# Kernel optimization log

Hardware: AMD Instinct MI355X
Metric: run time of the kernel (lower is better)

## Reference

```python
import jax, jax.numpy as jnp
import numpy as np

# CIM / quantization constants hardcoded in the source module
INPUT_BIT = 8
WEIGHT_BIT = 4
OUTPUT_BIT = 8
DAC_BIT = 2
ADC_BIT = 8
ADC_GAIN_1_SCALE = 1.0 / 63.0
GAIN_MIN, GAIN_MAX = 1.0, 255.0
N_SLICES = INPUT_BIT // DAC_BIT  # 4 bit-serial input slices of 2 bits each


def ste_round(v):
    # straight-through round: forward = round(v), backward = identity
    return v + jax.lax.stop_gradient(jnp.round(v) - v)


def conv2d(x, w):
    # NCHW conv, stride 1, padding k//2 (SAME for odd k)
    return jax.lax.conv_general_dilated(
        x, w, window_strides=(1, 1), padding='SAME',
        dimension_numbers=('NCHW', 'OIHW', 'NCHW'))


def setup_inputs() -> dict:
    key = jax.random.key(0)
    kx, kw, kb = jax.random.split(key, 3)
    B, Cin, H, W = 16, 4, 512, 512
    Cout, K = 8, 3
    x = jax.random.uniform(kx, (B, Cin, H, W), dtype=jnp.float32)  # non-negative activations
    weight = jax.random.normal(kw, (Cout, Cin, K, K), dtype=jnp.float32) * 0.05
    bias = jax.random.normal(kb, (Cout,), dtype=jnp.float32) * 0.01
    s_in = jnp.float32(1.0 / 255.0)   # LSQ input scale (8-bit unsigned)
    s_w = jnp.float32(0.02)           # LSQ weight scale (4-bit signed)
    s_out = jnp.float32(0.05)         # LSQ output scale (8-bit signed)
    return {"x": x, "weight": weight, "bias": bias,
            "s_in": s_in, "s_w": s_w, "s_out": s_out}


def reference(x, weight, bias, s_in, s_w, s_out):
    in_max = 2.0 ** INPUT_BIT - 1.0          # 255
    w_lim = 2.0 ** (WEIGHT_BIT - 1) - 1.0    # 7
    adc_max = 2.0 ** (ADC_BIT - 1) - 1.0     # 127
    o_lim = 2.0 ** (OUTPUT_BIT - 1) - 1.0    # 127
    base = float(2 ** DAC_BIT)               # 4 levels per DAC slice

    # LSQ quantization of input (unsigned) and weight (signed), STE rounding
    xq = jnp.clip(ste_round(x / s_in), 0.0, in_max)        # integer-valued floats
    wq = jnp.clip(ste_round(weight / s_w), -w_lim, w_lim)

    # ideal integer conv (gradient path)
    ideal = conv2d(xq, wq)

    # bit-serial DAC/ADC CIM path (forward only; noise_scale=0 so no noise)
    xi = jax.lax.stop_gradient(xq)
    wi = jax.lax.stop_gradient(wq)
    psums = []
    for s in range(N_SLICES):
        sl = jnp.mod(jnp.floor(xi / (base ** s)), base)    # 2-bit slice in [0,3]
        psums.append(conv2d(sl, wi))
    # ADC gain adjustment ('gain' mode): integer gain in [1,255], LSB = 1/(gain*gain_1_scale)
    p_absmax = jnp.maximum(
        jnp.max(jnp.stack([jnp.max(jnp.abs(p)) for p in psums])), 1e-6)
    gain = jnp.clip(jnp.round(adc_max / (p_absmax * ADC_GAIN_1_SCALE)),
                    GAIN_MIN, GAIN_MAX)
    step = 1.0 / (gain * ADC_GAIN_1_SCALE)
    acc = jnp.zeros_like(ideal)
    for s, p in enumerate(psums):
        adc_out = jnp.clip(jnp.round(p / step), -adc_max, adc_max) * step
        acc = acc + adc_out * (base ** s)

    # straight-through: forward uses analog path, backward uses ideal conv
    psum = ideal + jax.lax.stop_gradient(acc - ideal)

    out = psum * (s_in * s_w) + bias[None, :, None, None]
    # LSQ output quantization (8-bit signed)
    out = jnp.clip(ste_round(out / s_out), -o_lim, o_lim) * s_out
    return out
```

## Files before the change

### kernel.cpp

```cpp
#include <hip/hip_runtime.h>
#include <stdint.h>

#define B_   16
#define CIN  4
#define COUT 8
#define H_   512
#define W_   512
#define HP   (H_ + 2)
#define WP   (W_ + 2)
#define PMAX 756
#define TBL  (2 * PMAX + 1)
#define RPB  8
#define GY   (H_ / RPB)
#define NBLK (2 * GY * B_)
#define NQ   (B_ * HP)

__device__ __forceinline__ int dot4(uint32_t a, int b, int c) {
#if __has_builtin(__builtin_amdgcn_sdot4)
    return __builtin_amdgcn_sdot4((int)a, b, c, false);
#else
    int r = c;
#pragma unroll
    for (int i = 0; i < 4; ++i) {
        int av = (int)((a >> (8 * i)) & 0xFFu);
        int bv = ((int)(((uint32_t)b) << (24 - 8 * i))) >> 24;
        r += av * bv;
    }
    return r;
#endif
}

__device__ __forceinline__ int dot8(uint32_t a, int b, int c) {
#if __has_builtin(__builtin_amdgcn_sdot8)
    return __builtin_amdgcn_sdot8((int)a, b, c, false);
#else
    int r = c;
#pragma unroll
    for (int i = 0; i < 8; ++i) {
        int av = (int)((a >> (4 * i)) & 0xFu);
        int bv = ((int)(((uint32_t)b) << (28 - 4 * i))) >> 28;
        r += av * bv;
    }
    return r;
#endif
}

__device__ __forceinline__ float rfl_f(float v) {
    return __int_as_float(__builtin_amdgcn_readfirstlane(__float_as_int(v)));
}

__device__ __forceinline__ int wquant(const float* w, float s_w,
                                      int co, int ci, int tap) {
    const int kh = tap / 3, kw = tap % 3;
    float wv = w[((co * CIN + ci) * 3 + kh) * 3 + kw];
    float q  = rintf(__fdiv_rn(wv, s_w));
    q = fminf(fmaxf(q, -7.0f), 7.0f);
    return (int)q;
}

__global__ __launch_bounds__(128) void quant_pack_kernel(
        const float* __restrict__ x, const float* __restrict__ weight,
        const float* __restrict__ s_in_p, const float* __restrict__ s_w_p,
        uint32_t* __restrict__ xq, uint32_t* __restrict__ wq8,
        int* __restrict__ absmax) {
    const int raw = blockIdx.x;
    const int lin = (raw & 7) * (NQ / 8) + (raw >> 3);
    const int b = lin / HP, hp = lin % HP;
    const int t = threadIdx.x;
    if (raw == 0) {
        if (t == 0) *absmax = 0;
        const float s_w = *s_w_p;
        if (t < 32) {
            const int co = t >> 2, p = t & 3;
            const int tA = (p == 0) ? 0 : (p == 1) ? 3 : (p == 2) ? 6 : 2;
            const int tB = (p == 0) ? 1 : (p == 1) ? 4 : (p == 2) ? 7 : 5;
            uint32_t v = 0;
#pragma unroll
            for (int ci = 0; ci < CIN; ++ci) {
                v |= ((uint32_t)(wquant(weight, s_w, co, ci, tA) & 0xF)) << (8 * ci);
                v |= ((uint32_t)(wquant(weight, s_w, co, ci, tB) & 0xF)) << (8 * ci + 4);
            }
            wq8[t] = v;
        } else if (t < 40) {
            const int co = t - 32;
            uint32_t v = 0;
#pragma unroll
            for (int ci = 0; ci < CIN; ++ci)
                v |= ((uint32_t)(wquant(weight, s_w, co, ci, 8) & 0xFF)) << (8 * ci);
            wq8[32 + co] = v;
        }
    }
    uint32_t* dst = xq + ((size_t)b * HP + hp) * WP;
    if (hp == 0 || hp == HP - 1) {
        for (int i = t; i < WP; i += 128) dst[i] = 0;
        return;
    }
    const float s_in = *s_in_p;
    const int h = hp - 1;
    const size_t plane = (size_t)H_ * W_;
    const float* xr = x + ((size_t)b * CIN) * plane + (size_t)h * W_ + 4 * t;
    float4 v0 = *(const float4*)(xr);
    float4 v1 = *(const float4*)(xr + plane);
    float4 v2 = *(const float4*)(xr + 2 * plane);
    float4 v3 = *(const float4*)(xr + 3 * plane);
    uint32_t o0 = 0, o1 = 0, o2 = 0, o3 = 0;
#define QP(f, ci, oj)                                                  \
    { float q = rintf(__fdiv_rn((f), s_in));                           \
      q = fminf(fmaxf(q, 0.0f), 255.0f);                               \
      oj |= ((uint32_t)(int)q) << (8 * (ci)); }
    QP(v0.x, 0, o0) QP(v0.y, 0, o1) QP(v0.z, 0, o2) QP(v0.w, 0, o3)
    QP(v1.x, 1, o0) QP(v1.y, 1, o1) QP(v1.z, 1, o2) QP(v1.w, 1, o3)
    QP(v2.x, 2, o0) QP(v2.y, 2, o1) QP(v2.z, 2, o2) QP(v2.w, 2, o3)
    QP(v3.x, 3, o0) QP(v3.y, 3, o1) QP(v3.z, 3, o2) QP(v3.w, 3, o3)
#undef QP
    uint32_t* d = dst + 1 + 4 * t;
    d[0] = o0; d[1] = o1; d[2] = o2; d[3] = o3;
    if (t == 0) dst[0] = 0;
    if (t == 127) dst[WP - 1] = 0;
}

template <int PASS>
__global__ __launch_bounds__(256, 8) void conv_kernel(
        const uint32_t* __restrict__ xq, const uint32_t* __restrict__ wq8,
        const float* __restrict__ bias, const float* __restrict__ sp_in,
        const float* __restrict__ sp_w, const float* __restrict__ sp_out,
        int* __restrict__ absmax, float* __restrict__ out) {
    __shared__ float tbl[PASS == 2 ? TBL : 1];
    __shared__ int   red[PASS == 1 ? 4 : 1];
    const int tid = threadIdx.x;

    int w8s[32], w4s[8];
    {
        const int4* q4 = (const int4*)wq8;
#pragma unroll
        for (int i = 0; i < 8; ++i) {
            int4 w4i = q4[i];
            w8s[4 * i + 0] = __builtin_amdgcn_readfirstlane(w4i.x);
            w8s[4 * i + 1] = __builtin_amdgcn_readfirstlane(w4i.y);
            w8s[4 * i + 2] = __builtin_amdgcn_readfirstlane(w4i.z);
            w8s[4 * i + 3] = __builtin_amdgcn_readfirstlane(w4i.w);
        }
        int4 a0 = q4[8], a1 = q4[9];
        w4s[0] = __builtin_amdgcn_readfirstlane(a0.x);
        w4s[1] = __builtin_amdgcn_readfirstlane(a0.y);
        w4s[2] = __builtin_amdgcn_readfirstlane(a0.z);
        w4s[3] = __builtin_amdgcn_readfirstlane(a0.w);
        w4s[4] = __builtin_amdgcn_readfirstlane(a1.x);
        w4s[5] = __builtin_amdgcn_readfirstlane(a1.y);
        w4s[6] = __builtin_amdgcn_readfirstlane(a1.z);
        w4s[7] = __builtin_amdgcn_readfirstlane(a1.w);
    }

    float scale = 0.0f, s_out = 0.0f, br[COUT];
    if (PASS == 2) {
        const float pabs = fmaxf((float)(*absmax), 1e-6f);
        const float c63  = 1.0f / 63.0f;
        float g = rintf(__fdiv_rn(127.0f, __fmul_rn(pabs, c63)));
        g = fminf(fmaxf(g, 1.0f), 255.0f);
        const float step = __fdiv_rn(1.0f, __fmul_rn(g, c63));
        for (int i = tid; i < TBL; i += 256) {
            float p = (float)(i - PMAX);
            float r = rintf(__fdiv_rn(p, step));
            r = fminf(fmaxf(r, -127.0f), 127.0f);
            tbl[i] = __fmul_rn(r, step);
        }
        scale = __fmul_rn(rfl_f(*sp_in), rfl_f(*sp_w));
        s_out = rfl_f(*sp_out);
#pragma unroll
        for (int co = 0; co < COUT; ++co) br[co] = rfl_f(bias[co]);
        __syncthreads();
    }

    const int raw = blockIdx.x;
    const int lin = (raw & 7) * (NBLK / 8) + (raw >> 3);
    const int bx = lin & 1;
    const int hy = (lin >> 1) & (GY - 1);
    const int b  = lin >> 7;
    const int w0 = bx * 256 + tid;
    const int h0 = hy * RPB;

    const uint32_t* base = xq + ((size_t)b * HP + h0) * WP + w0;
    const size_t plane = (size_t)H_ * W_;

    uint32_t cpA[4][4];
    uint32_t sgl[4][4];

#define EXTROW(slot, v0, v1, v2)                                          \
    do {                                                                  \
        uint32_t lo = ((v0) & 0x0F0F0F0Fu) | (((v1) << 4) & 0xF0F0F0F0u); \
        uint32_t hi = (((v0) >> 4) & 0x0F0F0F0Fu) | ((v1) & 0xF0F0F0F0u); \
        cpA[slot][0] = lo & 0x33333333u;                                  \
        cpA[slot][1] = (lo >> 2) & 0x33333333u;                           \
        cpA[slot][2] = hi & 0x33333333u;                                  \
        cpA[slot][3] = (hi >> 2) & 0x33333333u;                           \
        sgl[slot][0] = (v2) & 0x03030303u;                                \
        sgl[slot][1] = ((v2) >> 2) & 0x03030303u;                         \
        sgl[slot][2] = ((v2) >> 4) & 0x03030303u;                         \
        sgl[slot][3] = ((v2) >> 6) & 0x03030303u;                         \
    } while (0)

    {
        uint32_t r0 = base[0], r1 = base[1], r2 = base[2];
        EXTROW(0, r0, r1, r2);
        r0 = base[WP]; r1 = base[WP + 1]; r2 = base[WP + 2];
        EXTROW(1, r0, r1, r2);
        r0 = base[2 * WP]; r1 = base[2 * WP + 1]; r2 = base[2 * WP + 2];
        EXTROW(2, r0, r1, r2);
    }
    uint32_t n0 = base[3 * WP], n1 = base[3 * WP + 1], n2 = base[3 * WP + 2];

    int runMax = 0, runMin = 0;

#pragma unroll
    for (int s = 0; s < RPB; ++s) {
        if (s >= 1) {
            EXTROW((s + 2) & 3, n0, n1, n2);
            if (s <= RPB - 2) {
                const uint32_t* nr = base + (size_t)(s + 3) * WP;
                n0 = nr[0]; n1 = nr[1]; n2 = nr[2];
            }
        }
        const int m0 = s & 3, m1 = (s + 1) & 3, m2 = (s + 2) & 3;

        uint32_t pc[4];
#pragma unroll
        for (int k = 0; k < 4; ++k) pc[k] = sgl[m0][k] | (sgl[m1][k] << 4);

        float* orow = (PASS == 2)
            ? out + ((size_t)b * COUT * H_ + (size_t)(h0 + s)) * W_ + w0
            : (float*)0;

#pragma unroll
        for (int co = 0; co < COUT; ++co) {
            float of = 0.0f;
#pragma unroll
            for (int k = 0; k < 4; ++k) {
                int a = dot4(sgl[m2][k], w4s[co], 0);
                a = dot8(cpA[m0][k], w8s[co * 4 + 0], a);
                a = dot8(cpA[m1][k], w8s[co * 4 + 1], a);
                a = dot8(cpA[m2][k], w8s[co * 4 + 2], a);
                a = dot8(pc[k],      w8s[co * 4 + 3], a);
                if (PASS == 1) {
                    runMax = max(runMax, a);
                    runMin = min(runMin, a);
                } else {
                    const float v = tbl[a + PMAX];
                    if (k == 0)      of = v;
                    else if (k == 1) of = __fadd_rn(of, __fmul_rn(v, 4.0f));
                    else if (k == 2) of = __fadd_rn(of, __fmul_rn(v, 16.0f));
                    else             of = __fadd_rn(of, __fmul_rn(v, 64.0f));
                }
            }
            if (PASS == 2) {
                float o = __fadd_rn(__fmul_rn(of, scale), br[co]);
                float q = rintf(__fdiv_rn(o, s_out));
                q = fminf(fmaxf(q, -127.0f), 127.0f);
                orow[(size_t)co * plane] = __fmul_rn(q, s_out);
            }
        }
    }
#undef EXTROW

    if (PASS == 1) {
        int m = max(runMax, -runMin);
#pragma unroll
        for (int off = 1; off < 64; off <<= 1)
            m = max(m, __shfl_xor(m, off));
        if ((tid & 63) == 0) red[tid >> 6] = m;
        __syncthreads();
        if (tid == 0) {
            int mm = max(max(red[0], red[1]), max(red[2], red[3]));
            atomicMax(absmax, mm);
        }
    }
}

extern "C" void kernel_launch(void* const* d_in, const int* in_sizes, int n_in,
                              void* d_out, int out_size, void* d_ws, size_t ws_size,
                              hipStream_t stream) {
    const float* x      = (const float*)d_in[0];
    const float* weight = (const float*)d_in[1];
    const float* bias   = (const float*)d_in[2];
    const float* s_in   = (const float*)d_in[3];
    const float* s_w    = (const float*)d_in[4];
    const float* s_out  = (const float*)d_in[5];
    float* out = (float*)d_out;

    int*      absmax = (int*)d_ws;
    uint32_t* wq8    = (uint32_t*)((char*)d_ws + 256);
    uint32_t* xq     = (uint32_t*)((char*)d_ws + 1024);

    quant_pack_kernel<<<dim3(NQ), dim3(128), 0, stream>>>(
        x, weight, s_in, s_w, xq, wq8, absmax);

    conv_kernel<1><<<dim3(NBLK), dim3(256), 0, stream>>>(
        xq, wq8, bias, s_in, s_w, s_out, absmax, out);
    conv_kernel<2><<<dim3(NBLK), dim3(256), 0, stream>>>(
        xq, wq8, bias, s_in, s_w, s_out, absmax, out);
}
```

Measured before the change: 99.10 us.

## Fuse input quantization with first conv pass using LDS tiles

Merges the quantize/pack kernel and the absmax conv pass into one kernel. Each block quantizes a haloed 10-row tile into LDS, writes the packed rows to the workspace for the second pass, and computes the absmax conv directly from LDS. This drops a kernel launch and the global re-read of packed inputs in pass one. In exchange, halo pixels are quantized redundantly, strided scalar loads of x replace float4 loads, and a memset is added to reset absmax.

```diff
diff --git a/kernel.cpp b/kernel.cpp
--- a/kernel.cpp
+++ b/kernel.cpp
@@ -13,7 +13,7 @@
 #define RPB  8
 #define GY   (H_ / RPB)
 #define NBLK (2 * GY * B_)
-#define NQ   (B_ * HP)
+#define LCOL 264
 
 __device__ __forceinline__ int dot4(uint32_t a, int b, int c) {
 #if __has_builtin(__builtin_amdgcn_sdot4)
@@ -58,75 +58,162 @@
     return (int)q;
 }
 
-__global__ __launch_bounds__(128) void quant_pack_kernel(
+__device__ __forceinline__ uint32_t qpix(const float* __restrict__ x,
+                                         float s_in, int b, int d, int c) {
+    const size_t plane = (size_t)H_ * W_;
+    const float* p = x + ((size_t)b * CIN) * plane + (size_t)d * W_ + c;
+    uint32_t v = 0;
+#pragma unroll
+    for (int ci = 0; ci < CIN; ++ci) {
+        float q = rintf(__fdiv_rn(p[ci * plane], s_in));
+        q = fminf(fmaxf(q, 0.0f), 255.0f);
+        v |= ((uint32_t)(int)q) << (8 * ci);
+    }
+    return v;
+}
+
+#define EXTROW(slot, v0, v1, v2)                                          \
+    do {                                                                  \
+        uint32_t lo = ((v0) & 0x0F0F0F0Fu) | (((v1) << 4) & 0xF0F0F0F0u); \
+        uint32_t hi = (((v0) >> 4) & 0x0F0F0F0Fu) | ((v1) & 0xF0F0F0F0u); \
+        cpA[slot][0] = lo & 0x33333333u;                                  \
+        cpA[slot][1] = (lo >> 2) & 0x33333333u;                           \
+        cpA[slot][2] = (hi)&0x33333333u;                                  \
+        cpA[slot][3] = (hi >> 2) & 0x33333333u;                           \
+        sgl[slot][0] = (v2)&0x03030303u;                                  \
+        sgl[slot][1] = ((v2) >> 2) & 0x03030303u;                         \
+        sgl[slot][2] = ((v2) >> 4) & 0x03030303u;                         \
+        sgl[slot][3] = ((v2) >> 6) & 0x03030303u;                         \
+    } while (0)
+
+__global__ __launch_bounds__(256, 8) void quant_conv1(
         const float* __restrict__ x, const float* __restrict__ weight,
         const float* __restrict__ s_in_p, const float* __restrict__ s_w_p,
         uint32_t* __restrict__ xq, uint32_t* __restrict__ wq8,
         int* __restrict__ absmax) {
+    __shared__ uint32_t lds[10][LCOL];
+    __shared__ uint32_t wlds[40];
+    __shared__ int      red[4];
+    const int t = threadIdx.x;
+
     const int raw = blockIdx.x;
-    const int lin = (raw & 7) * (NQ / 8) + (raw >> 3);
-    const int b = lin / HP, hp = lin % HP;
-    const int t = threadIdx.x;
-    if (raw == 0) {
-        if (t == 0) *absmax = 0;
+    const int lin = (raw & 7) * (NBLK / 8) + (raw >> 3);
+    const int bx = lin & 1;
+    const int hy = (lin >> 1) & (GY - 1);
+    const int b  = lin >> 7;
+    const int w0 = bx * 256;
+    const int h0 = hy * RPB;
+
+    const float s_in = *s_in_p;
+
+    if (t < 40) {
         const float s_w = *s_w_p;
+        uint32_t v = 0;
         if (t < 32) {
             const int co = t >> 2, p = t & 3;
             const int tA = (p == 0) ? 0 : (p == 1) ? 3 : (p == 2) ? 6 : 2;
             const int tB = (p == 0) ? 1 : (p == 1) ? 4 : (p == 2) ? 7 : 5;
-            uint32_t v = 0;
 #pragma unroll
             for (int ci = 0; ci < CIN; ++ci) {
                 v |= ((uint32_t)(wquant(weight, s_w, co, ci, tA) & 0xF)) << (8 * ci);
                 v |= ((uint32_t)(wquant(weight, s_w, co, ci, tB) & 0xF)) << (8 * ci + 4);
             }
-            wq8[t] = v;
-        } else if (t < 40) {
+        } else {
             const int co = t - 32;
-            uint32_t v = 0;
 #pragma unroll
             for (int ci = 0; ci < CIN; ++ci)
                 v |= ((uint32_t)(wquant(weight, s_w, co, ci, 8) & 0xFF)) << (8 * ci);
-            wq8[32 + co] = v;
-        }
-    }
-    uint32_t* dst = xq + ((size_t)b * HP + hp) * WP;
-    if (hp == 0 || hp == HP - 1) {
-        for (int i = t; i < WP; i += 128) dst[i] = 0;
-        return;
-    }
-    const float s_in = *s_in_p;
-    const int h = hp - 1;
-    const size_t plane = (size_t)H_ * W_;
-    const float* xr = x + ((size_t)b * CIN) * plane + (size_t)h * W_ + 4 * t;
-    float4 v0 = *(const float4*)(xr);
-    float4 v1 = *(const float4*)(xr + plane);
-    float4 v2 = *(const float4*)(xr + 2 * plane);
-    float4 v3 = *(const float4*)(xr + 3 * plane);
-    uint32_t o0 = 0, o1 = 0, o2 = 0, o3 = 0;
-#define QP(f, ci, oj)                                                  \
-    { float q = rintf(__fdiv_rn((f), s_in));                           \
-      q = fminf(fmaxf(q, 0.0f), 255.0f);                               \
-      oj |= ((uint32_t)(int)q) << (8 * (ci)); }
-    QP(v0.x, 0, o0) QP(v0.y, 0, o1) QP(v0.z, 0, o2) QP(v0.w, 0, o3)
-    QP(v1.x, 1, o0) QP(v1.y, 1, o1) QP(v1.z, 1, o2) QP(v1.w, 1, o3)
-    QP(v2.x, 2, o0) QP(v2.y, 2, o1) QP(v2.z, 2, o2) QP(v2.w, 2, o3)
-    QP(v3.x, 3, o0) QP(v3.y, 3, o1) QP(v3.z, 3, o2) QP(v3.w, 3, o3)
-#undef QP
-    uint32_t* d = dst + 1 + 4 * t;
-    d[0] = o0; d[1] = o1; d[2] = o2; d[3] = o3;
-    if (t == 0) dst[0] = 0;
-    if (t == 127) dst[WP - 1] = 0;
-}
-
-template <int PASS>
-__global__ __launch_bounds__(256, 8) void conv_kernel(
+        }
+        wlds[t] = v;
+        if (raw == 0) wq8[t] = v;
+    }
+
+#pragma unroll 2
+    for (int r = 0; r < 10; ++r) {
+        const int d = h0 - 1 + r;
+        const bool rowok = ((unsigned)d < (unsigned)H_);
+        const int c = w0 - 1 + t;
+        uint32_t v = 0;
+        if (rowok && (unsigned)c < (unsigned)W_) v = qpix(x, s_in, b, d, c);
+        lds[r][t] = v;
+        if (t < 2) {
+            const int c2 = w0 + 255 + t;
+            uint32_t v2 = 0;
+            if (rowok && (unsigned)c2 < (unsigned)W_) v2 = qpix(x, s_in, b, d, c2);
+            lds[r][256 + t] = v2;
+        }
+    }
+    __syncthreads();
+
+    {
+        uint32_t* xb = xq + (size_t)b * HP * WP;
+#pragma unroll
+        for (int r = 1; r <= 8; ++r)
+            xb[(size_t)(h0 + r) * WP + (w0 + 1 + t)] = lds[r][t + 1];
+        if (hy == 0)
+            for (int i = t; i < WP; i += 256) xb[i] = 0;
+        if (hy == GY - 1)
+            for (int i = t; i < WP; i += 256) xb[(size_t)(HP - 1) * WP + i] = 0;
+        if (t == 0) {
+            const int col = (bx == 0) ? 0 : (WP - 1);
+#pragma unroll
+            for (int r = 1; r <= 8; ++r) xb[(size_t)(h0 + r) * WP + col] = 0;
+        }
+    }
+
+    int w8s[32], w4s[8];
+#pragma unroll
+    for (int i = 0; i < 32; ++i)
+        w8s[i] = __builtin_amdgcn_readfirstlane((int)wlds[i]);
+#pragma unroll
+    for (int i = 0; i < 8; ++i)
+        w4s[i] = __builtin_amdgcn_readfirstlane((int)wlds[32 + i]);
+
+    uint32_t cpA[4][4], sgl[4][4];
+    EXTROW(0, lds[0][t], lds[0][t + 1], lds[0][t + 2]);
+    EXTROW(1, lds[1][t], lds[1][t + 1], lds[1][t + 2]);
+
+    int runMax = 0, runMin = 0;
+#pragma unroll
+    for (int s = 0; s < RPB; ++s) {
+        EXTROW((s + 2) & 3, lds[s + 2][t], lds[s + 2][t + 1], lds[s + 2][t + 2]);
+        const int m0 = s & 3, m1 = (s + 1) & 3, m2 = (s + 2) & 3;
+        uint32_t pc[4];
+#pragma unroll
+        for (int k = 0; k < 4; ++k) pc[k] = sgl[m0][k] | (sgl[m1][k] << 4);
+#pragma unroll
+        for (int co = 0; co < COUT; ++co) {
+#pragma unroll
+            for (int k = 0; k < 4; ++k) {
+                int a = dot4(sgl[m2][k], w4s[co], 0);
+                a = dot8(cpA[m0][k], w8s[co * 4 + 0], a);
+                a = dot8(cpA[m1][k], w8s[co * 4 + 1], a);
+                a = dot8(cpA[m2][k], w8s[co * 4 + 2], a);
+                a = dot8(pc[k],      w8s[co * 4 + 3], a);
+                runMax = max(runMax, a);
+                runMin = min(runMin, a);
+            }
+        }
+    }
+
+    int m = max(runMax, -runMin);
+#pragma unroll
+    for (int off = 1; off < 64; off <<= 1)
+        m = max(m, __shfl_xor(m, off));
+    if ((t & 63) == 0) red[t >> 6] = m;
+    __syncthreads();
+    if (t == 0) {
+        int mm = max(max(red[0], red[1]), max(red[2], red[3]));
+        atomicMax(absmax, mm);
+    }
+}
+
+__global__ __launch_bounds__(256, 8) void conv2_kernel(
         const uint32_t* __restrict__ xq, const uint32_t* __restrict__ wq8,
         const float* __restrict__ bias, const float* __restrict__ sp_in,
         const float* __restrict__ sp_w, const float* __restrict__ sp_out,
         int* __restrict__ absmax, float* __restrict__ out) {
-    __shared__ float tbl[PASS == 2 ? TBL : 1];
-    __shared__ int   red[PASS == 1 ? 4 : 1];
+    __shared__ float tbl[TBL];
     const int tid = threadIdx.x;
 
     int w8s[32], w4s[8];
@@ -151,25 +238,23 @@
         w4s[7] = __builtin_amdgcn_readfirstlane(a1.w);
     }
 
-    float scale = 0.0f, s_out = 0.0f, br[COUT];
-    if (PASS == 2) {
-        const float pabs = fmaxf((float)(*absmax), 1e-6f);
-        const float c63  = 1.0f / 63.0f;
-        float g = rintf(__fdiv_rn(127.0f, __fmul_rn(pabs, c63)));
-        g = fminf(fmaxf(g, 1.0f), 255.0f);
-        const float step = __fdiv_rn(1.0f, __fmul_rn(g, c63));
-        for (int i = tid; i < TBL; i += 256) {
-            float p = (float)(i - PMAX);
-            float r = rintf(__fdiv_rn(p, step));
-            r = fminf(fmaxf(r, -127.0f), 127.0f);
-            tbl[i] = __fmul_rn(r, step);
-        }
-        scale = __fmul_rn(rfl_f(*sp_in), rfl_f(*sp_w));
-        s_out = rfl_f(*sp_out);
-#pragma unroll
-        for (int co = 0; co < COUT; ++co) br[co] = rfl_f(bias[co]);
-        __syncthreads();
-    }
+    const float pabs = fmaxf((float)(*absmax), 1e-6f);
+    const float c63  = 1.0f / 63.0f;
+    float g = rintf(__fdiv_rn(127.0f, __fmul_rn(pabs, c63)));
+    g = fminf(fmaxf(g, 1.0f), 255.0f);
+    const float step = __fdiv_rn(1.0f, __fmul_rn(g, c63));
+    for (int i = tid; i < TBL; i += 256) {
+        float p = (float)(i - PMAX);
+        float r = rintf(__fdiv_rn(p, step));
+        r = fminf(fmaxf(r, -127.0f), 127.0f);
+        tbl[i] = __fmul_rn(r, step);
+    }
+    const float scale = __fmul_rn(rfl_f(*sp_in), rfl_f(*sp_w));
+    const float s_out = rfl_f(*sp_out);
+    float br[COUT];
+#pragma unroll
+    for (int co = 0; co < COUT; ++co) br[co] = rfl_f(bias[co]);
+    __syncthreads();
 
     const int raw = blockIdx.x;
     const int lin = (raw & 7) * (NBLK / 8) + (raw >> 3);
@@ -182,54 +267,28 @@
     const uint32_t* base = xq + ((size_t)b * HP + h0) * WP + w0;
     const size_t plane = (size_t)H_ * W_;
 
-    uint32_t cpA[4][4];
-    uint32_t sgl[4][4];
-
-#define EXTROW(slot, v0, v1, v2)                                          \
-    do {                                                                  \
-        uint32_t lo = ((v0) & 0x0F0F0F0Fu) | (((v1) << 4) & 0xF0F0F0F0u); \
-        uint32_t hi = (((v0) >> 4) & 0x0F0F0F0Fu) | ((v1) & 0xF0F0F0F0u); \
-        cpA[slot][0] = lo & 0x33333333u;                                  \
-        cpA[slot][1] = (lo >> 2) & 0x33333333u;                           \
-        cpA[slot][2] = hi & 0x33333333u;                                  \
-        cpA[slot][3] = (hi >> 2) & 0x33333333u;                           \
-        sgl[slot][0] = (v2) & 0x03030303u;                                \
-        sgl[slot][1] = ((v2) >> 2) & 0x03030303u;                         \
-        sgl[slot][2] = ((v2) >> 4) & 0x03030303u;                         \
-        sgl[slot][3] = ((v2) >> 6) & 0x03030303u;                         \
-    } while (0)
-
+    uint32_t cpA[4][4], sgl[4][4];
     {
         uint32_t r0 = base[0], r1 = base[1], r2 = base[2];
         EXTROW(0, r0, r1, r2);
         r0 = base[WP]; r1 = base[WP + 1]; r2 = base[WP + 2];
         EXTROW(1, r0, r1, r2);
-        r0 = base[2 * WP]; r1 = base[2 * WP + 1]; r2 = base[2 * WP + 2];
-        EXTROW(2, r0, r1, r2);
-    }
-    uint32_t n0 = base[3 * WP], n1 = base[3 * WP + 1], n2 = base[3 * WP + 2];
-
-    int runMax = 0, runMin = 0;
+    }
+    uint32_t n0 = base[2 * WP], n1 = base[2 * WP + 1], n2 = base[2 * WP + 2];
 
 #pragma unroll
     for (int s = 0; s < RPB; ++s) {
-        if (s >= 1) {
-            EXTROW((s + 2) & 3, n0, n1, n2);
-            if (s <= RPB - 2) {
-                const uint32_t* nr = base + (size_t)(s + 3) * WP;
-                n0 = nr[0]; n1 = nr[1]; n2 = nr[2];
-            }
+        EXTROW((s + 2) & 3, n0, n1, n2);
+        if (s <= RPB - 2) {
+            const uint32_t* nr = base + (size_t)(s + 3) * WP;
+            n0 = nr[0]; n1 = nr[1]; n2 = nr[2];
         }
         const int m0 = s & 3, m1 = (s + 1) & 3, m2 = (s + 2) & 3;
-
         uint32_t pc[4];
 #pragma unroll
         for (int k = 0; k < 4; ++k) pc[k] = sgl[m0][k] | (sgl[m1][k] << 4);
 
-        float* orow = (PASS == 2)
-            ? out + ((size_t)b * COUT * H_ + (size_t)(h0 + s)) * W_ + w0
-            : (float*)0;
-
+        float* orow = out + ((size_t)b * COUT * H_ + (size_t)(h0 + s)) * W_ + w0;
 #pragma unroll
         for (int co = 0; co < COUT; ++co) {
             float of = 0.0f;
@@ -240,37 +299,16 @@
                 a = dot8(cpA[m1][k], w8s[co * 4 + 1], a);
                 a = dot8(cpA[m2][k], w8s[co * 4 + 2], a);
                 a = dot8(pc[k],      w8s[co * 4 + 3], a);
-                if (PASS == 1) {
-                    runMax = max(runMax, a);
-                    runMin = min(runMin, a);
-                } else {
-                    const float v = tbl[a + PMAX];
-                    if (k == 0)      of = v;
-                    else if (k == 1) of = __fadd_rn(of, __fmul_rn(v, 4.0f));
-                    else if (k == 2) of = __fadd_rn(of, __fmul_rn(v, 16.0f));
-                    else             of = __fadd_rn(of, __fmul_rn(v, 64.0f));
-                }
+                const float v = tbl[a + PMAX];
+                if (k == 0)      of = v;
+                else if (k == 1) of = __fadd_rn(of, __fmul_rn(v, 4.0f));
+                else if (k == 2) of = __fadd_rn(of, __fmul_rn(v, 16.0f));
+                else             of = __fadd_rn(of, __fmul_rn(v, 64.0f));
             }
-            if (PASS == 2) {
-                float o = __fadd_rn(__fmul_rn(of, scale), br[co]);
-                float q = rintf(__fdiv_rn(o, s_out));
-                q = fminf(fmaxf(q, -127.0f), 127.0f);
-                orow[(size_t)co * plane] = __fmul_rn(q, s_out);
-            }
-        }
-    }
-#undef EXTROW
-
-    if (PASS == 1) {
-        int m = max(runMax, -runMin);
-#pragma unroll
-        for (int off = 1; off < 64; off <<= 1)
-            m = max(m, __shfl_xor(m, off));
-        if ((tid & 63) == 0) red[tid >> 6] = m;
-        __syncthreads();
-        if (tid == 0) {
-            int mm = max(max(red[0], red[1]), max(red[2], red[3]));
-            atomicMax(absmax, mm);
+            float o = __fadd_rn(__fmul_rn(of, scale), br[co]);
+            float q = rintf(__fdiv_rn(o, s_out));
+            q = fminf(fmaxf(q, -127.0f), 127.0f);
+            orow[(size_t)co * plane] = __fmul_rn(q, s_out);
         }
     }
 }
@@ -290,11 +328,11 @@
     uint32_t* wq8    = (uint32_t*)((char*)d_ws + 256);
     uint32_t* xq     = (uint32_t*)((char*)d_ws + 1024);
 
-    quant_pack_kernel<<<dim3(NQ), dim3(128), 0, stream>>>(
+    hipMemsetAsync(absmax, 0, sizeof(int), stream);
+
+    quant_conv1<<<dim3(NBLK), dim3(256), 0, stream>>>(
         x, weight, s_in, s_w, xq, wq8, absmax);
 
-    conv_kernel<1><<<dim3(NBLK), dim3(256), 0, stream>>>(
+    conv2_kernel<<<dim3(NBLK), dim3(256), 0, stream>>>(
         xq, wq8, bias, s_in, s_w, s_out, absmax, out);
-    conv_kernel<2><<<dim3(NBLK), dim3(256), 0, stream>>>(
-        xq, wq8, bias, s_in, s_w, s_out, absmax, out);
-}
+}
```

Measured after the change: 118.1 us. +19.2%, slower.
